# Optimization experiments

Hardware: AMD Instinct MI355X
Metric: run time of the kernel (lower is better)

Reference implementation:

```python
import jax, jax.numpy as jnp
import numpy as np

KEY_DIM = 64
DENSE_DIM = 128
B, N, M = 8, 2048, 256


def setup_inputs() -> dict:
    key = jax.random.key(0)
    ks = jax.random.split(key, 10)
    s_in = 1.0 / np.sqrt(M)
    s_k = 1.0 / np.sqrt(KEY_DIM)
    s_d = 1.0 / np.sqrt(DENSE_DIM)
    return {
        "x": jax.random.normal(ks[0], (B, N, M), dtype=jnp.float32),
        "Wq": jax.random.normal(ks[1], (M, KEY_DIM), dtype=jnp.float32) * s_in,
        "Wk": jax.random.normal(ks[2], (M, KEY_DIM), dtype=jnp.float32) * s_in,
        "Wv": jax.random.normal(ks[3], (M, KEY_DIM), dtype=jnp.float32) * s_in,
        "W1": jax.random.normal(ks[4], (KEY_DIM, DENSE_DIM), dtype=jnp.float32) * s_k,
        "b1": jnp.zeros((DENSE_DIM,), dtype=jnp.float32),
        "W2": jax.random.normal(ks[5], (DENSE_DIM, DENSE_DIM), dtype=jnp.float32) * s_d,
        "b2": jnp.zeros((DENSE_DIM,), dtype=jnp.float32),
        "W3": jax.random.normal(ks[6], (DENSE_DIM, DENSE_DIM), dtype=jnp.float32) * s_d,
        "b3": jnp.zeros((DENSE_DIM,), dtype=jnp.float32),
    }


def reference(x, Wq, Wk, Wv, W1, b1, W2, b2, W3, b3):
    scale = np.sqrt(KEY_DIM).astype(np.float32)
    q = jnp.einsum('bnm,mk->bnk', x, Wq)
    k = jnp.einsum('bnm,mk->bnk', x, Wk)
    v = jnp.einsum('bnm,mk->bnk', x, Wv)
    scores = jnp.einsum('bik,bjk->bij', q, k) / scale  # [B, N, N]
    weights = jax.nn.softmax(scores, axis=-1)
    z = jnp.einsum('bij,bjk->bik', weights, v)  # [B, N, key_dim]
    h = jax.nn.elu(z @ W1 + b1)
    h = jax.nn.elu(h @ W2 + b2)
    out = jax.nn.elu(h @ W3 + b3)
    return out
```

## Files before the change

### kernel.cpp

```cpp
#include <hip/hip_runtime.h>
#include <cstdint>
#include <cstddef>

#define B_ 8
#define N_ 2048
#define M_ 256
#define KD 64
#define DD 128
#define BN (B_ * N_)
#define KSPLIT 4
#define KT_PER (N_ / 64 / KSPLIT)

typedef __attribute__((ext_vector_type(8))) short s16x8;
typedef __attribute__((ext_vector_type(4))) float f32x4;
typedef __attribute__((ext_vector_type(4))) unsigned int u32x4;

__device__ __forceinline__ float elu_f(float x) {
    return x > 0.f ? x : (__expf(x) - 1.f);
}

__device__ __forceinline__ unsigned short f2bf(float f) {
    unsigned int u = __float_as_uint(f);
    u = (u + 0x7FFFu + ((u >> 16) & 1u)) >> 16;
    return (unsigned short)u;
}
__device__ __forceinline__ float bf2f(unsigned short h) {
    return __uint_as_float((unsigned int)h << 16);
}
__device__ __forceinline__ unsigned short bflo(float f, unsigned short h) {
    return f2bf(f - bf2f(h));
}
__device__ __forceinline__ unsigned int packw(float f) {
    unsigned short h = f2bf(f);
    unsigned short lo = bflo(f, h);
    return (unsigned int)h | ((unsigned int)lo << 16);
}
__device__ __forceinline__ unsigned int bfpack2(float a, float b) {
    return (unsigned int)f2bf(a) | ((unsigned int)f2bf(b) << 16);
}

__device__ __forceinline__ void unpack8(const unsigned int* ip, s16x8& ahi, s16x8& alo) {
    const uint4 u0 = *reinterpret_cast<const uint4*>(ip);
    const uint4 u1 = *reinterpret_cast<const uint4*>(ip + 4);
    u32x4 hv, lv;
    hv.x = __byte_perm(u0.x, u0.y, 0x5410);
    hv.y = __byte_perm(u0.z, u0.w, 0x5410);
    hv.z = __byte_perm(u1.x, u1.y, 0x5410);
    hv.w = __byte_perm(u1.z, u1.w, 0x5410);
    lv.x = __byte_perm(u0.x, u0.y, 0x7632);
    lv.y = __byte_perm(u0.z, u0.w, 0x7632);
    lv.z = __byte_perm(u1.x, u1.y, 0x7632);
    lv.w = __byte_perm(u1.z, u1.w, 0x7632);
    ahi = __builtin_bit_cast(s16x8, hv);
    alo = __builtin_bit_cast(s16x8, lv);
}

__global__ __launch_bounds__(256)
void pack_kernel(const float* __restrict__ Wq, const float* __restrict__ Wk,
                 const float* __restrict__ Wv, const float* __restrict__ W1,
                 const float* __restrict__ W2, const float* __restrict__ W3,
                 unsigned short* __restrict__ pQh, unsigned short* __restrict__ pQl,
                 unsigned short* __restrict__ pW1h, unsigned short* __restrict__ pW1l,
                 unsigned short* __restrict__ pW2h, unsigned short* __restrict__ pW2l,
                 unsigned short* __restrict__ pW3h, unsigned short* __restrict__ pW3l) {
    const int id = blockIdx.x * 256 + threadIdx.x;
    const float* W;
    unsigned short *ph, *pl;
    int ncol, ct, c, lane, base;
    if (id < 6144) {
        int mat = id >> 11, rem = id & 2047;
        ct = rem >> 9; c = (rem >> 6) & 7; lane = rem & 63;
        W = (mat == 0) ? Wq : (mat == 1) ? Wk : Wv;
        ncol = KD; ph = pQh; pl = pQl;
        base = (((mat * 4 + ct) * 8 + c) * 64 + lane) * 8;
    } else {
        int id2 = id - 6144;
        if (id2 < 1024) {
            ct = id2 >> 7; c = (id2 >> 6) & 1; lane = id2 & 63;
            W = W1; ncol = DD; ph = pW1h; pl = pW1l;
            base = ((ct * 2 + c) * 64 + lane) * 8;
        } else if (id2 < 3072) {
            int id3 = id2 - 1024;
            ct = id3 >> 8; c = (id3 >> 6) & 3; lane = id3 & 63;
            W = W2; ncol = DD; ph = pW2h; pl = pW2l;
            base = ((ct * 4 + c) * 64 + lane) * 8;
        } else {
            int id3 = id2 - 3072;
            ct = id3 >> 8; c = (id3 >> 6) & 3; lane = id3 & 63;
            W = W3; ncol = DD; ph = pW3h; pl = pW3l;
            base = ((ct * 4 + c) * 64 + lane) * 8;
        }
    }
    const int col = ct * 16 + (lane & 15);
    const int kb = c * 32 + (lane >> 4) * 8;
    #pragma unroll
    for (int j = 0; j < 8; ++j) {
        float v = W[(size_t)(kb + j) * ncol + col];
        unsigned short h = f2bf(v);
        ph[base + j] = h;
        pl[base + j] = bflo(v, h);
    }
}

__global__ __launch_bounds__(256)
void qkv_kernel(const float* __restrict__ x,
                const unsigned short* __restrict__ pQh,
                unsigned short* __restrict__ qb, unsigned short* __restrict__ kb,
                unsigned short* __restrict__ vtb) {
    __shared__ unsigned short xh[32 * 264];
    __shared__ float dbuf[32 * 204];
    const int t = threadIdx.x;
    const int row0 = blockIdx.x * 32;

    for (int i = t; i < 2048; i += 256) {
        int rr = i >> 6, c4 = i & 63;
        float4 v = reinterpret_cast<const float4*>(x + (size_t)(row0 + rr) * M_)[c4];
        ushort4 o;
        o.x = f2bf(v.x); o.y = f2bf(v.y); o.z = f2bf(v.z); o.w = f2bf(v.w);
        *reinterpret_cast<ushort4*>(&xh[rr * 264 + c4 * 4]) = o;
    }
    __syncthreads();

    const int w = t >> 6, l = t & 63, g = l >> 4, r = l & 15;
    const int t0 = 3 * w, t1 = 3 * w + 1, t2 = 3 * w + 2;

    f32x4 acc[3][2];
    #pragma unroll
    for (int m = 0; m < 3; ++m)
        #pragma unroll
        for (int s = 0; s < 2; ++s)
            acc[m][s] = (f32x4){0.f, 0.f, 0.f, 0.f};

    #pragma unroll
    for (int c = 0; c < 8; ++c) {
        const s16x8 a0 = *reinterpret_cast<const s16x8*>(&xh[r * 264 + c * 32 + g * 8]);
        const s16x8 a1 = *reinterpret_cast<const s16x8*>(&xh[(16 + r) * 264 + c * 32 + g * 8]);
        const s16x8 b0 = *reinterpret_cast<const s16x8*>(pQh + ((t0 * 8 + c) * 64 + l) * 8);
        const s16x8 b1 = *reinterpret_cast<const s16x8*>(pQh + ((t1 * 8 + c) * 64 + l) * 8);
        const s16x8 b2 = *reinterpret_cast<const s16x8*>(pQh + ((t2 * 8 + c) * 64 + l) * 8);
        acc[0][0] = __builtin_amdgcn_mfma_f32_16x16x32_bf16(a0, b0, acc[0][0], 0, 0, 0);
        acc[0][1] = __builtin_amdgcn_mfma_f32_16x16x32_bf16(a1, b0, acc[0][1], 0, 0, 0);
        acc[1][0] = __builtin_amdgcn_mfma_f32_16x16x32_bf16(a0, b1, acc[1][0], 0, 0, 0);
        acc[1][1] = __builtin_amdgcn_mfma_f32_16x16x32_bf16(a1, b1, acc[1][1], 0, 0, 0);
        acc[2][0] = __builtin_amdgcn_mfma_f32_16x16x32_bf16(a0, b2, acc[2][0], 0, 0, 0);
        acc[2][1] = __builtin_amdgcn_mfma_f32_16x16x32_bf16(a1, b2, acc[2][1], 0, 0, 0);
    }

    {
        const int c0 = (t0 >> 2) * 68 + (t0 & 3) * 16 + r;
        const int c1 = (t1 >> 2) * 68 + (t1 & 3) * 16 + r;
        const int c2 = (t2 >> 2) * 68 + (t2 & 3) * 16 + r;
        #pragma unroll
        for (int s = 0; s < 2; ++s)
            #pragma unroll
            for (int reg = 0; reg < 4; ++reg) {
                const int rw = (s * 16 + 4 * g + reg) * 204;
                dbuf[rw + c0] = acc[0][s][reg];
                dbuf[rw + c1] = acc[1][s][reg];
                dbuf[rw + c2] = acc[2][s][reg];
            }
    }
    __syncthreads();

    const int b = row0 >> 11, n0 = row0 & 2047;
    {
        const int mat = t >> 7, rem = t & 127, rr = rem >> 2, cq = rem & 3;
        const float* src = &dbuf[rr * 204 + mat * 68 + cq * 16];
        float4 v0 = *reinterpret_cast<const float4*>(src);
        float4 v1 = *reinterpret_cast<const float4*>(src + 4);
        float4 v2 = *reinterpret_cast<const float4*>(src + 8);
        float4 v3 = *reinterpret_cast<const float4*>(src + 12);
        const float sc = (mat == 0) ? 0.125f : 1.0f;
        uint4 o0, o1;
        o0.x = bfpack2(v0.x * sc, v0.y * sc);
        o0.y = bfpack2(v0.z * sc, v0.w * sc);
        o0.z = bfpack2(v1.x * sc, v1.y * sc);
        o0.w = bfpack2(v1.z * sc, v1.w * sc);
        o1.x = bfpack2(v2.x * sc, v2.y * sc);
        o1.y = bfpack2(v2.z * sc, v2.w * sc);
        o1.z = bfpack2(v3.x * sc, v3.y * sc);
        o1.w = bfpack2(v3.z * sc, v3.w * sc);
        unsigned short* dst = (mat == 0 ? qb : kb) + (size_t)(row0 + rr) * KD + cq * 16;
        *reinterpret_cast<uint4*>(dst)     = o0;
        *reinterpret_cast<uint4*>(dst + 8) = o1;
    }
    {
        const int d = t >> 2, ng = (t & 3) * 8;
        unsigned short tmp[8];
        #pragma unroll
        for (int i = 0; i < 8; ++i)
            tmp[i] = f2bf(dbuf[(ng + i) * 204 + 136 + d]);
        uint4 o0;
        o0.x = (unsigned)tmp[0] | ((unsigned)tmp[1] << 16);
        o0.y = (unsigned)tmp[2] | ((unsigned)tmp[3] << 16);
        o0.z = (unsigned)tmp[4] | ((unsigned)tmp[5] << 16);
        o0.w = (unsigned)tmp[6] | ((unsigned)tmp[7] << 16);
        *reinterpret_cast<uint4*>(vtb + ((size_t)b * KD + d) * N_ + n0 + ng) = o0;
    }
}

__global__ __launch_bounds__(128)
void attn_kernel(const unsigned short* __restrict__ qb,
                 const unsigned short* __restrict__ kb,
                 const unsigned short* __restrict__ vtb,
                 float* __restrict__ Zp, float* __restrict__ lsum) {
    __shared__ __align__(16) unsigned short ks[64 * 72];
    __shared__ __align__(16) unsigned short vt[64 * 72];
    __shared__ __align__(16) unsigned short ps[2 * 32 * 72];

    const int t = threadIdx.x;
    const int w = t >> 6;
    const int l = t & 63;
    const int g = l >> 4;
    const int r = l & 15;
    const int bid = blockIdx.x;
    const int split = bid & 3;
    const int qt = (bid >> 2) & 31;
    const int bb = bid >> 7;
    const int qrow0 = qt * 64 + w * 32;
    const int k0 = split * (N_ / KSPLIT);

    const unsigned short* qrowA = qb + ((size_t)bb * N_ + qrow0 + r) * KD + g * 8;
    const unsigned short* qrowB = qrowA + (size_t)16 * KD;
    const s16x8 qfA0 = *reinterpret_cast<const s16x8*>(qrowA);
    const s16x8 qfA1 = *reinterpret_cast<const s16x8*>(qrowA + 32);
    const s16x8 qfB0 = *reinterpret_cast<const s16x8*>(qrowB);
    const s16x8 qfB1 = *reinterpret_cast<const s16x8*>(qrowB + 32);

    const unsigned short* kbase = kb + ((size_t)bb * N_ + k0) * KD;
    const unsigned short* vbase = vtb + (size_t)bb * KD * N_ + k0;
    unsigned short* psw = ps + w * (32 * 72);

    for (int c = t; c < 512; c += 128) {
        int key = c >> 3, sub = c & 7;
        *reinterpret_cast<s16x8*>(&ks[key * 72 + sub * 8]) =
            *reinterpret_cast<const s16x8*>(kbase + (size_t)key * KD + sub * 8);
        *reinterpret_cast<s16x8*>(&vt[key * 72 + sub * 8]) =
            *reinterpret_cast<const s16x8*>(vbase + (size_t)key * N_ + sub * 8);
    }
    __syncthreads();

    f32x4 zacA0 = {0.f,0.f,0.f,0.f}, zacA1 = {0.f,0.f,0.f,0.f};
    f32x4 zacA2 = {0.f,0.f,0.f,0.f}, zacA3 = {0.f,0.f,0.f,0.f};
    f32x4 zacB0 = {0.f,0.f,0.f,0.f}, zacB1 = {0.f,0.f,0.f,0.f};
    f32x4 zacB2 = {0.f,0.f,0.f,0.f}, zacB3 = {0.f,0.f,0.f,0.f};
    float laccA[4] = {0.f, 0.f, 0.f, 0.f};
    float laccB[4] = {0.f, 0.f, 0.f, 0.f};

    for (int kt = 0; kt < KT_PER; ++kt) {
        s16x8 kr[4], vr[4];
        const bool pf = (kt + 1 < KT_PER);
        if (pf) {
            const unsigned short* kg = kbase + (size_t)(kt + 1) * 64 * KD;
            const unsigned short* vg = vbase + (size_t)(kt + 1) * 64;
            #pragma unroll
            for (int i = 0; i < 4; ++i) {
                const int c = t + 128 * i, key = c >> 3, sub = c & 7;
                kr[i] = *reinterpret_cast<const s16x8*>(kg + (size_t)key * KD + sub * 8);
                vr[i] = *reinterpret_cast<const s16x8*>(vg + (size_t)key * N_ + sub * 8);
            }
        }

        f32x4 sA0 = {0.f,0.f,0.f,0.f}, sA1 = {0.f,0.f,0.f,0.f};
        f32x4 sA2 = {0.f,0.f,0.f,0.f}, sA3 = {0.f,0.f,0.f,0.f};
        f32x4 sB0 = {0.f,0.f,0.f,0.f}, sB1 = {0.f,0.f,0.f,0.f};
        f32x4 sB2 = {0.f,0.f,0.f,0.f}, sB3 = {0.f,0.f,0.f,0.f};
        {
            const s16x8 kf00 = *reinterpret_cast<const s16x8*>(&ks[(r +  0) * 72 + g * 8]);
            const s16x8 kf01 = *reinterpret_cast<const s16x8*>(&ks[(r +  0) * 72 + g * 8 + 32]);
            const s16x8 kf10 = *reinterpret_cast<const s16x8*>(&ks[(r + 16) * 72 + g * 8]);
            const s16x8 kf11 = *reinterpret_cast<const s16x8*>(&ks[(r + 16) * 72 + g * 8 + 32]);
            const s16x8 kf20 = *reinterpret_cast<const s16x8*>(&ks[(r + 32) * 72 + g * 8]);
            const s16x8 kf21 = *reinterpret_cast<const s16x8*>(&ks[(r + 32) * 72 + g * 8 + 32]);
            const s16x8 kf30 = *reinterpret_cast<const s16x8*>(&ks[(r + 48) * 72 + g * 8]);
            const s16x8 kf31 = *reinterpret_cast<const s16x8*>(&ks[(r + 48) * 72 + g * 8 + 32]);
            sA0 = __builtin_amdgcn_mfma_f32_16x16x32_bf16(qfA0, kf00, sA0, 0, 0, 0);
            sA0 = __builtin_amdgcn_mfma_f32_16x16x32_bf16(qfA1, kf01, sA0, 0, 0, 0);
            sA1 = __builtin_amdgcn_mfma_f32_16x16x32_bf16(qfA0, kf10, sA1, 0, 0, 0);
            sA1 = __builtin_amdgcn_mfma_f32_16x16x32_bf16(qfA1, kf11, sA1, 0, 0, 0);
            sA2 = __builtin_amdgcn_mfma_f32_16x16x32_bf16(qfA0, kf20, sA2, 0, 0, 0);
            sA2 = __builtin_amdgcn_mfma_f32_16x16x32_bf16(qfA1, kf21, sA2, 0, 0, 0);
            sA3 = __builtin_amdgcn_mfma_f32_16x16x32_bf16(qfA0, kf30, sA3, 0, 0, 0);
            sA3 = __builtin_amdgcn_mfma_f32_16x16x32_bf16(qfA1, kf31, sA3, 0, 0, 0);
            sB0 = __builtin_amdgcn_mfma_f32_16x16x32_bf16(qfB0, kf00, sB0, 0, 0, 0);
            sB0 = __builtin_amdgcn_mfma_f32_16x16x32_bf16(qfB1, kf01, sB0, 0, 0, 0);
            sB1 = __builtin_amdgcn_mfma_f32_16x16x32_bf16(qfB0, kf10, sB1, 0, 0, 0);
            sB1 = __builtin_amdgcn_mfma_f32_16x16x32_bf16(qfB1, kf11, sB1, 0, 0, 0);
            sB2 = __builtin_amdgcn_mfma_f32_16x16x32_bf16(qfB0, kf20, sB2, 0, 0, 0);
            sB2 = __builtin_amdgcn_mfma_f32_16x16x32_bf16(qfB1, kf21, sB2, 0, 0, 0);
            sB3 = __builtin_amdgcn_mfma_f32_16x16x32_bf16(qfB0, kf30, sB3, 0, 0, 0);
            sB3 = __builtin_amdgcn_mfma_f32_16x16x32_bf16(qfB1, kf31, sB3, 0, 0, 0);
        }

        const s16x8 vf00 = *reinterpret_cast<const s16x8*>(&vt[(r +  0) * 72 + g * 8]);
        const s16x8 vf01 = *reinterpret_cast<const s16x8*>(&vt[(r +  0) * 72 + g * 8 + 32]);
        const s16x8 vf10 = *reinterpret_cast<const s16x8*>(&vt[(r + 16) * 72 + g * 8]);
        const s16x8 vf11 = *reinterpret_cast<const s16x8*>(&vt[(r + 16) * 72 + g * 8 + 32]);
        const s16x8 vf20 = *reinterpret_cast<const s16x8*>(&vt[(r + 32) * 72 + g * 8]);
        const s16x8 vf21 = *reinterpret_cast<const s16x8*>(&vt[(r + 32) * 72 + g * 8 + 32]);
        const s16x8 vf30 = *reinterpret_cast<const s16x8*>(&vt[(r + 48) * 72 + g * 8]);
        const s16x8 vf31 = *reinterpret_cast<const s16x8*>(&vt[(r + 48) * 72 + g * 8 + 32]);

        #pragma unroll
        for (int j = 0; j < 4; ++j) {
            float p0 = __expf(sA0[j]);
            float p1 = __expf(sA1[j]);
            float p2 = __expf(sA2[j]);
            float p3 = __expf(sA3[j]);
            laccA[j] += (p0 + p1) + (p2 + p3);
            psw[(4 * g + j) * 72 + r +  0] = f2bf(p0);
            psw[(4 * g + j) * 72 + r + 16] = f2bf(p1);
            psw[(4 * g + j) * 72 + r + 32] = f2bf(p2);
            psw[(4 * g + j) * 72 + r + 48] = f2bf(p3);
        }
        #pragma unroll
        for (int j = 0; j < 4; ++j) {
            float p0 = __expf(sB0[j]);
            float p1 = __expf(sB1[j]);
            float p2 = __expf(sB2[j]);
            float p3 = __expf(sB3[j]);
            laccB[j] += (p0 + p1) + (p2 + p3);
            psw[(16 + 4 * g + j) * 72 + r +  0] = f2bf(p0);
            psw[(16 + 4 * g + j) * 72 + r + 16] = f2bf(p1);
            psw[(16 + 4 * g + j) * 72 + r + 32] = f2bf(p2);
            psw[(16 + 4 * g + j) * 72 + r + 48] = f2bf(p3);
        }

        asm volatile("s_waitcnt lgkmcnt(0)" ::: "memory");
        __builtin_amdgcn_sched_barrier(0);

        const s16x8 paA0 = *reinterpret_cast<const s16x8*>(&psw[r * 72 + g * 8]);
        const s16x8 paA1 = *reinterpret_cast<const s16x8*>(&psw[r * 72 + g * 8 + 32]);
        const s16x8 paB0 = *reinterpret_cast<const s16x8*>(&psw[(16 + r) * 72 + g * 8]);
        const s16x8 paB1 = *reinterpret_cast<const s16x8*>(&psw[(16 + r) * 72 + g * 8 + 32]);
        zacA0 = __builtin_amdgcn_mfma_f32_16x16x32_bf16(paA0, vf00, zacA0, 0, 0, 0);
        zacA0 = __builtin_amdgcn_mfma_f32_16x16x32_bf16(paA1, vf01, zacA0, 0, 0, 0);
        zacA1 = __builtin_amdgcn_mfma_f32_16x16x32_bf16(paA0, vf10, zacA1, 0, 0, 0);
        zacA1 = __builtin_amdgcn_mfma_f32_16x16x32_bf16(paA1, vf11, zacA1, 0, 0, 0);
        zacA2 = __builtin_amdgcn_mfma_f32_16x16x32_bf16(paA0, vf20, zacA2, 0, 0, 0);
        zacA2 = __builtin_amdgcn_mfma_f32_16x16x32_bf16(paA1, vf21, zacA2, 0, 0, 0);
        zacA3 = __builtin_amdgcn_mfma_f32_16x16x32_bf16(paA0, vf30, zacA3, 0, 0, 0);
        zacA3 = __builtin_amdgcn_mfma_f32_16x16x32_bf16(paA1, vf31, zacA3, 0, 0, 0);
        zacB0 = __builtin_amdgcn_mfma_f32_16x16x32_bf16(paB0, vf00, zacB0, 0, 0, 0);
        zacB0 = __builtin_amdgcn_mfma_f32_16x16x32_bf16(paB1, vf01, zacB0, 0, 0, 0);
        zacB1 = __builtin_amdgcn_mfma_f32_16x16x32_bf16(paB0, vf10, zacB1, 0, 0, 0);
        zacB1 = __builtin_amdgcn_mfma_f32_16x16x32_bf16(paB1, vf11, zacB1, 0, 0, 0);
        zacB2 = __builtin_amdgcn_mfma_f32_16x16x32_bf16(paB0, vf20, zacB2, 0, 0, 0);
        zacB2 = __builtin_amdgcn_mfma_f32_16x16x32_bf16(paB1, vf21, zacB2, 0, 0, 0);
        zacB3 = __builtin_amdgcn_mfma_f32_16x16x32_bf16(paB0, vf30, zacB3, 0, 0, 0);
        zacB3 = __builtin_amdgcn_mfma_f32_16x16x32_bf16(paB1, vf31, zacB3, 0, 0, 0);

        __syncthreads();
        if (pf) {
            #pragma unroll
            for (int i = 0; i < 4; ++i) {
                const int c = t + 128 * i, key = c >> 3, sub = c & 7;
                *reinterpret_cast<s16x8*>(&ks[key * 72 + sub * 8]) = kr[i];
                *reinterpret_cast<s16x8*>(&vt[key * 72 + sub * 8]) = vr[i];
            }
        }
        __syncthreads();
    }

    const size_t rowbase = (size_t)split * BN + (size_t)bb * N_ + qrow0;
    #pragma unroll
    for (int j = 0; j < 4; ++j) {
        float lt = laccA[j];
        lt += __shfl_xor(lt, 1);
        lt += __shfl_xor(lt, 2);
        lt += __shfl_xor(lt, 4);
        lt += __shfl_xor(lt, 8);
        if (r == 0)
            lsum[rowbase + 4 * g + j] = lt;
        float* zr = Zp + (rowbase + 4 * g + j) * KD + r;
        zr[ 0] = zacA0[j];
        zr[16] = zacA1[j];
        zr[32] = zacA2[j];
        zr[48] = zacA3[j];
    }
    #pragma unroll
    for (int j = 0; j < 4; ++j) {
        float lt = laccB[j];
        lt += __shfl_xor(lt, 1);
        lt += __shfl_xor(lt, 2);
        lt += __shfl_xor(lt, 4);
        lt += __shfl_xor(lt, 8);
        if (r == 0)
            lsum[rowbase + 16 + 4 * g + j] = lt;
        float* zr = Zp + (rowbase + 16 + 4 * g + j) * KD + r;
        zr[ 0] = zacB0[j];
        zr[16] = zacB1[j];
        zr[32] = zacB2[j];
        zr[48] = zacB3[j];
    }
}

__global__ __launch_bounds__(256)
void mlp_kernel(const float* __restrict__ Zp, const float* __restrict__ lsum,
                const unsigned short* __restrict__ pW1h, const unsigned short* __restrict__ pW1l,
                const unsigned short* __restrict__ pW2h, const unsigned short* __restrict__ pW2l,
                const unsigned short* __restrict__ pW3h, const unsigned short* __restrict__ pW3l,
                const float* __restrict__ b1, const float* __restrict__ b2,
                const float* __restrict__ b3, float* __restrict__ out) {
    __shared__ unsigned int zW[32 * 68];
    __shared__ unsigned int hW[32 * 140];
    const int t = threadIdx.x;
    const int row0 = blockIdx.x * 32;

    {
        const int rr = t >> 3, c8 = (t & 7) * 8;
        const size_t grow = (size_t)row0 + rr;
        const float inv = 1.0f / (lsum[grow] + lsum[BN + grow] +
                                  lsum[2 * (size_t)BN + grow] + lsum[3 * (size_t)BN + grow]);
        const size_t off = grow * KD + c8;
        uint4 wv0, wv1;
        {
            float4 a0 = *reinterpret_cast<const float4*>(Zp + off);
            float4 a1 = *reinterpret_cast<const float4*>(Zp + (size_t)BN * KD + off);
            float4 a2 = *reinterpret_cast<const float4*>(Zp + 2 * (size_t)BN * KD + off);
            float4 a3 = *reinterpret_cast<const float4*>(Zp + 3 * (size_t)BN * KD + off);
            wv0.x = packw((a0.x + a1.x + a2.x + a3.x) * inv);
            wv0.y = packw((a0.y + a1.y + a2.y + a3.y) * inv);
            wv0.z = packw((a0.z + a1.z + a2.z + a3.z) * inv);
            wv0.w = packw((a0.w + a1.w + a2.w + a3.w) * inv);
        }
        {
            float4 a0 = *reinterpret_cast<const float4*>(Zp + off + 4);
            float4 a1 = *reinterpret_cast<const float4*>(Zp + (size_t)BN * KD + off + 4);
            float4 a2 = *reinterpret_cast<const float4*>(Zp + 2 * (size_t)BN * KD + off + 4);
            float4 a3 = *reinterpret_cast<const float4*>(Zp + 3 * (size_t)BN * KD + off + 4);
            wv1.x = packw((a0.x + a1.x + a2.x + a3.x) * inv);
            wv1.y = packw((a0.y + a1.y + a2.y + a3.y) * inv);
            wv1.z = packw((a0.z + a1.z + a2.z + a3.z) * inv);
            wv1.w = packw((a0.w + a1.w + a2.w + a3.w) * inv);
        }
        *reinterpret_cast<uint4*>(&zW[rr * 68 + c8])     = wv0;
        *reinterpret_cast<uint4*>(&zW[rr * 68 + c8 + 4]) = wv1;
    }
    __syncthreads();

    const int w = t >> 6, l = t & 63, g = l >> 4, r = l & 15;
    const int ctA = 2 * w, ctB = 2 * w + 1;

    f32x4 aA[2], aB[2];
    #pragma unroll
    for (int s = 0; s < 2; ++s) { aA[s] = (f32x4){0,0,0,0}; aB[s] = (f32x4){0,0,0,0}; }
    #pragma unroll
    for (int c = 0; c < 2; ++c) {
        s16x8 h0, l0, h1, l1;
        unpack8(&zW[r * 68 + c * 32 + g * 8], h0, l0);
        unpack8(&zW[(16 + r) * 68 + c * 32 + g * 8], h1, l1);
        const int baseA = ((ctA * 2 + c) * 64 + l) * 8;
        const int baseB = ((ctB * 2 + c) * 64 + l) * 8;
        const s16x8 bhA = *reinterpret_cast<const s16x8*>(pW1h + baseA);
        const s16x8 blA = *reinterpret_cast<const s16x8*>(pW1l + baseA);
        const s16x8 bhB = *reinterpret_cast<const s16x8*>(pW1h + baseB);
        const s16x8 blB = *reinterpret_cast<const s16x8*>(pW1l + baseB);
        aA[0] = __builtin_amdgcn_mfma_f32_16x16x32_bf16(h0, bhA, aA[0], 0, 0, 0);
        aA[0] = __builtin_amdgcn_mfma_f32_16x16x32_bf16(h0, blA, aA[0], 0, 0, 0);
        aA[0] = __builtin_amdgcn_mfma_f32_16x16x32_bf16(l0, bhA, aA[0], 0, 0, 0);
        aA[1] = __builtin_amdgcn_mfma_f32_16x16x32_bf16(h1, bhA, aA[1], 0, 0, 0);
        aA[1] = __builtin_amdgcn_mfma_f32_16x16x32_bf16(h1, blA, aA[1], 0, 0, 0);
        aA[1] = __builtin_amdgcn_mfma_f32_16x16x32_bf16(l1, bhA, aA[1], 0, 0, 0);
        aB[0] = __builtin_amdgcn_mfma_f32_16x16x32_bf16(h0, bhB, aB[0], 0, 0, 0);
        aB[0] = __builtin_amdgcn_mfma_f32_16x16x32_bf16(h0, blB, aB[0], 0, 0, 0);
        aB[0] = __builtin_amdgcn_mfma_f32_16x16x32_bf16(l0, bhB, aB[0], 0, 0, 0);
        aB[1] = __builtin_amdgcn_mfma_f32_16x16x32_bf16(h1, bhB, aB[1], 0, 0, 0);
        aB[1] = __builtin_amdgcn_mfma_f32_16x16x32_bf16(h1, blB, aB[1], 0, 0, 0);
        aB[1] = __builtin_amdgcn_mfma_f32_16x16x32_bf16(l1, bhB, aB[1], 0, 0, 0);
    }
    {
        const float bvA = b1[ctA * 16 + r], bvB = b1[ctB * 16 + r];
        #pragma unroll
        for (int s = 0; s < 2; ++s)
            #pragma unroll
            for (int reg = 0; reg < 4; ++reg) {
                const int rw = (s * 16 + 4 * g + reg) * 140;
                hW[rw + ctA * 16 + r] = packw(elu_f(aA[s][reg] + bvA));
                hW[rw + ctB * 16 + r] = packw(elu_f(aB[s][reg] + bvB));
            }
    }
    __syncthreads();

    #pragma unroll
    for (int s = 0; s < 2; ++s) { aA[s] = (f32x4){0,0,0,0}; aB[s] = (f32x4){0,0,0,0}; }
    #pragma unroll
    for (int c = 0; c < 4; ++c) {
        s16x8 h0, l0, h1, l1;
        unpack8(&hW[r * 140 + c * 32 + g * 8], h0, l0);
        unpack8(&hW[(16 + r) * 140 + c * 32 + g * 8], h1, l1);
        const int baseA = ((ctA * 4 + c) * 64 + l) * 8;
        const int baseB = ((ctB * 4 + c) * 64 + l) * 8;
        const s16x8 bhA = *reinterpret_cast<const s16x8*>(pW2h + baseA);
        const s16x8 blA = *reinterpret_cast<const s16x8*>(pW2l + baseA);
        const s16x8 bhB = *reinterpret_cast<const s16x8*>(pW2h + baseB);
        const s16x8 blB = *reinterpret_cast<const s16x8*>(pW2l + baseB);
        aA[0] = __builtin_amdgcn_mfma_f32_16x16x32_bf16(h0, bhA, aA[0], 0, 0, 0);
        aA[0] = __builtin_amdgcn_mfma_f32_16x16x32_bf16(h0, blA, aA[0], 0, 0, 0);
        aA[0] = __builtin_amdgcn_mfma_f32_16x16x32_bf16(l0, bhA, aA[0], 0, 0, 0);
        aA[1] = __builtin_amdgcn_mfma_f32_16x16x32_bf16(h1, bhA, aA[1], 0, 0, 0);
        aA[1] = __builtin_amdgcn_mfma_f32_16x16x32_bf16(h1, blA, aA[1], 0, 0, 0);
        aA[1] = __builtin_amdgcn_mfma_f32_16x16x32_bf16(l1, bhA, aA[1], 0, 0, 0);
        aB[0] = __builtin_amdgcn_mfma_f32_16x16x32_bf16(h0, bhB, aB[0], 0, 0, 0);
        aB[0] = __builtin_amdgcn_mfma_f32_16x16x32_bf16(h0, blB, aB[0], 0, 0, 0);
        aB[0] = __builtin_amdgcn_mfma_f32_16x16x32_bf16(l0, bhB, aB[0], 0, 0, 0);
        aB[1] = __builtin_amdgcn_mfma_f32_16x16x32_bf16(h1, bhB, aB[1], 0, 0, 0);
        aB[1] = __builtin_amdgcn_mfma_f32_16x16x32_bf16(h1, blB, aB[1], 0, 0, 0);
        aB[1] = __builtin_amdgcn_mfma_f32_16x16x32_bf16(l1, bhB, aB[1], 0, 0, 0);
    }
    __syncthreads();
    {
        const float bvA = b2[ctA * 16 + r], bvB = b2[ctB * 16 + r];
        #pragma unroll
        for (int s = 0; s < 2; ++s)
            #pragma unroll
            for (int reg = 0; reg < 4; ++reg) {
                const int rw = (s * 16 + 4 * g + reg) * 140;
                hW[rw + ctA * 16 + r] = packw(elu_f(aA[s][reg] + bvA));
                hW[rw + ctB * 16 + r] = packw(elu_f(aB[s][reg] + bvB));
            }
    }
    __syncthreads();

    #pragma unroll
    for (int s = 0; s < 2; ++s) { aA[s] = (f32x4){0,0,0,0}; aB[s] = (f32x4){0,0,0,0}; }
    #pragma unroll
    for (int c = 0; c < 4; ++c) {
        s16x8 h0, l0, h1, l1;
        unpack8(&hW[r * 140 + c * 32 + g * 8], h0, l0);
        unpack8(&hW[(16 + r) * 140 + c * 32 + g * 8], h1, l1);
        const int baseA = ((ctA * 4 + c) * 64 + l) * 8;
        const int baseB = ((ctB * 4 + c) * 64 + l) * 8;
        const s16x8 bhA = *reinterpret_cast<const s16x8*>(pW3h + baseA);
        const s16x8 blA = *reinterpret_cast<const s16x8*>(pW3l + baseA);
        const s16x8 bhB = *reinterpret_cast<const s16x8*>(pW3h + baseB);
        const s16x8 blB = *reinterpret_cast<const s16x8*>(pW3l + baseB);
        aA[0] = __builtin_amdgcn_mfma_f32_16x16x32_bf16(h0, bhA, aA[0], 0, 0, 0);
        aA[0] = __builtin_amdgcn_mfma_f32_16x16x32_bf16(h0, blA, aA[0], 0, 0, 0);
        aA[0] = __builtin_amdgcn_mfma_f32_16x16x32_bf16(l0, bhA, aA[0], 0, 0, 0);
        aA[1] = __builtin_amdgcn_mfma_f32_16x16x32_bf16(h1, bhA, aA[1], 0, 0, 0);
        aA[1] = __builtin_amdgcn_mfma_f32_16x16x32_bf16(h1, blA, aA[1], 0, 0, 0);
        aA[1] = __builtin_amdgcn_mfma_f32_16x16x32_bf16(l1, bhA, aA[1], 0, 0, 0);
        aB[0] = __builtin_amdgcn_mfma_f32_16x16x32_bf16(h0, bhB, aB[0], 0, 0, 0);
        aB[0] = __builtin_amdgcn_mfma_f32_16x16x32_bf16(h0, blB, aB[0], 0, 0, 0);
        aB[0] = __builtin_amdgcn_mfma_f32_16x16x32_bf16(l0, bhB, aB[0], 0, 0, 0);
        aB[1] = __builtin_amdgcn_mfma_f32_16x16x32_bf16(h1, bhB, aB[1], 0, 0, 0);
        aB[1] = __builtin_amdgcn_mfma_f32_16x16x32_bf16(h1, blB, aB[1], 0, 0, 0);
        aB[1] = __builtin_amdgcn_mfma_f32_16x16x32_bf16(l1, bhB, aB[1], 0, 0, 0);
    }
    {
        const float bvA = b3[ctA * 16 + r], bvB = b3[ctB * 16 + r];
        #pragma unroll
        for (int s = 0; s < 2; ++s)
            #pragma unroll
            for (int reg = 0; reg < 4; ++reg) {
                float* orow = out + (size_t)(row0 + s * 16 + 4 * g + reg) * DD;
                orow[ctA * 16 + r] = elu_f(aA[s][reg] + bvA);
                orow[ctB * 16 + r] = elu_f(aB[s][reg] + bvB);
            }
    }
}

extern "C" void kernel_launch(void* const* d_in, const int* in_sizes, int n_in,
                              void* d_out, int out_size, void* d_ws, size_t ws_size,
                              hipStream_t stream) {
    (void)in_sizes; (void)n_in; (void)out_size; (void)ws_size;
    const float* x  = (const float*)d_in[0];
    const float* Wq = (const float*)d_in[1];
    const float* Wk = (const float*)d_in[2];
    const float* Wv = (const float*)d_in[3];
    const float* W1 = (const float*)d_in[4];
    const float* b1 = (const float*)d_in[5];
    const float* W2 = (const float*)d_in[6];
    const float* b2 = (const float*)d_in[7];
    const float* W3 = (const float*)d_in[8];
    const float* b3 = (const float*)d_in[9];
    float* out = (float*)d_out;

    const size_t nt = (size_t)BN * KD;
    unsigned short* qbf = (unsigned short*)d_ws;
    unsigned short* kbf = qbf + nt;
    unsigned short* vtb = kbf + nt;
    float* Zp   = (float*)(vtb + nt);
    float* lsum = Zp + (size_t)KSPLIT * nt;
    unsigned short* pQh  = (unsigned short*)(lsum + (size_t)KSPLIT * BN);
    unsigned short* pQl  = pQh + 49152;
    unsigned short* pW1h = pQl + 49152;
    unsigned short* pW1l = pW1h + 8192;
    unsigned short* pW2h = pW1l + 8192;
    unsigned short* pW2l = pW2h + 16384;
    unsigned short* pW3h = pW2l + 16384;
    unsigned short* pW3l = pW3h + 16384;

    pack_kernel<<<dim3(44), 256, 0, stream>>>(Wq, Wk, Wv, W1, W2, W3,
                                              pQh, pQl, pW1h, pW1l, pW2h, pW2l, pW3h, pW3l);
    qkv_kernel<<<dim3(BN / 32), 256, 0, stream>>>(x, pQh, qbf, kbf, vtb);
    attn_kernel<<<dim3(BN / 64 * KSPLIT), 128, 0, stream>>>(qbf, kbf, vtb, Zp, lsum);
    mlp_kernel<<<dim3(BN / 32), 256, 0, stream>>>(Zp, lsum, pW1h, pW1l, pW2h, pW2l,
                                                  pW3h, pW3l, b1, b2, b3, out);
}
```

Before: 55.02 us.

## Keep softmax probabilities in registers via transposed QK^T and store bf16 partials

The QK^T MFMA operands are swapped so each lane's score accumulator already matches the A-operand layout needed for the PV MFMA. The probabilities are packed to bf16 in registers instead of going through a shared-memory round trip. The V tile is stored with a permuted column slot order to match this register layout. The split-K partial Z outputs are written as bf16 rather than fp32, halving partial-sum traffic into the MLP kernel, at the cost of some precision in the accumulated partials.

```diff
diff --git a/kernel.cpp b/kernel.cpp
--- a/kernel.cpp
+++ b/kernel.cpp
@@ -38,6 +38,8 @@
 __device__ __forceinline__ unsigned int bfpack2(float a, float b) {
     return (unsigned int)f2bf(a) | ((unsigned int)f2bf(b) << 16);
 }
+__device__ __forceinline__ float bflo32(unsigned int u) { return __uint_as_float(u << 16); }
+__device__ __forceinline__ float bfhi32(unsigned int u) { return __uint_as_float(u & 0xffff0000u); }
 
 __device__ __forceinline__ void unpack8(const unsigned int* ip, s16x8& ahi, s16x8& alo) {
     const uint4 u0 = *reinterpret_cast<const uint4*>(ip);
@@ -203,10 +205,9 @@
 void attn_kernel(const unsigned short* __restrict__ qb,
                  const unsigned short* __restrict__ kb,
                  const unsigned short* __restrict__ vtb,
-                 float* __restrict__ Zp, float* __restrict__ lsum) {
+                 unsigned short* __restrict__ Zp, float* __restrict__ lsum) {
     __shared__ __align__(16) unsigned short ks[64 * 72];
     __shared__ __align__(16) unsigned short vt[64 * 72];
-    __shared__ __align__(16) unsigned short ps[2 * 32 * 72];
 
     const int t = threadIdx.x;
     const int w = t >> 6;
@@ -229,14 +230,16 @@
 
     const unsigned short* kbase = kb + ((size_t)bb * N_ + k0) * KD;
     const unsigned short* vbase = vtb + (size_t)bb * KD * N_ + k0;
-    unsigned short* psw = ps + w * (32 * 72);
 
     for (int c = t; c < 512; c += 128) {
-        int key = c >> 3, sub = c & 7;
-        *reinterpret_cast<s16x8*>(&ks[key * 72 + sub * 8]) =
-            *reinterpret_cast<const s16x8*>(kbase + (size_t)key * KD + sub * 8);
-        *reinterpret_cast<s16x8*>(&vt[key * 72 + sub * 8]) =
-            *reinterpret_cast<const s16x8*>(vbase + (size_t)key * N_ + sub * 8);
+        const int row = c >> 3, sub = c & 7;
+        *reinterpret_cast<s16x8*>(&ks[row * 72 + sub * 8]) =
+            *reinterpret_cast<const s16x8*>(kbase + (size_t)row * KD + sub * 8);
+        const s16x8 vv = *reinterpret_cast<const s16x8*>(vbase + (size_t)row * N_ + sub * 8);
+        const u32x4 vw = __builtin_bit_cast(u32x4, vv);
+        const int slot = 32 * (sub >> 2) + 16 * (sub & 1) + 4 * ((sub >> 1) & 1);
+        *reinterpret_cast<uint2*>(&vt[row * 72 + slot])     = make_uint2(vw.x, vw.y);
+        *reinterpret_cast<uint2*>(&vt[row * 72 + slot + 8]) = make_uint2(vw.z, vw.w);
     }
     __syncthreads();
 
@@ -244,8 +247,7 @@
     f32x4 zacA2 = {0.f,0.f,0.f,0.f}, zacA3 = {0.f,0.f,0.f,0.f};
     f32x4 zacB0 = {0.f,0.f,0.f,0.f}, zacB1 = {0.f,0.f,0.f,0.f};
     f32x4 zacB2 = {0.f,0.f,0.f,0.f}, zacB3 = {0.f,0.f,0.f,0.f};
-    float laccA[4] = {0.f, 0.f, 0.f, 0.f};
-    float laccB[4] = {0.f, 0.f, 0.f, 0.f};
+    float laccA = 0.f, laccB = 0.f;
 
     for (int kt = 0; kt < KT_PER; ++kt) {
         s16x8 kr[4], vr[4];
@@ -255,16 +257,15 @@
             const unsigned short* vg = vbase + (size_t)(kt + 1) * 64;
             #pragma unroll
             for (int i = 0; i < 4; ++i) {
-                const int c = t + 128 * i, key = c >> 3, sub = c & 7;
-                kr[i] = *reinterpret_cast<const s16x8*>(kg + (size_t)key * KD + sub * 8);
-                vr[i] = *reinterpret_cast<const s16x8*>(vg + (size_t)key * N_ + sub * 8);
+                const int c = t + 128 * i, row = c >> 3, sub = c & 7;
+                kr[i] = *reinterpret_cast<const s16x8*>(kg + (size_t)row * KD + sub * 8);
+                vr[i] = *reinterpret_cast<const s16x8*>(vg + (size_t)row * N_ + sub * 8);
             }
         }
 
-        f32x4 sA0 = {0.f,0.f,0.f,0.f}, sA1 = {0.f,0.f,0.f,0.f};
-        f32x4 sA2 = {0.f,0.f,0.f,0.f}, sA3 = {0.f,0.f,0.f,0.f};
-        f32x4 sB0 = {0.f,0.f,0.f,0.f}, sB1 = {0.f,0.f,0.f,0.f};
-        f32x4 sB2 = {0.f,0.f,0.f,0.f}, sB3 = {0.f,0.f,0.f,0.f};
+        f32x4 sA[4], sB[4];
+        #pragma unroll
+        for (int i = 0; i < 4; ++i) { sA[i] = (f32x4){0,0,0,0}; sB[i] = (f32x4){0,0,0,0}; }
         {
             const s16x8 kf00 = *reinterpret_cast<const s16x8*>(&ks[(r +  0) * 72 + g * 8]);
             const s16x8 kf01 = *reinterpret_cast<const s16x8*>(&ks[(r +  0) * 72 + g * 8 + 32]);
@@ -274,23 +275,53 @@
             const s16x8 kf21 = *reinterpret_cast<const s16x8*>(&ks[(r + 32) * 72 + g * 8 + 32]);
             const s16x8 kf30 = *reinterpret_cast<const s16x8*>(&ks[(r + 48) * 72 + g * 8]);
             const s16x8 kf31 = *reinterpret_cast<const s16x8*>(&ks[(r + 48) * 72 + g * 8 + 32]);
-            sA0 = __builtin_amdgcn_mfma_f32_16x16x32_bf16(qfA0, kf00, sA0, 0, 0, 0);
-            sA0 = __builtin_amdgcn_mfma_f32_16x16x32_bf16(qfA1, kf01, sA0, 0, 0, 0);
-            sA1 = __builtin_amdgcn_mfma_f32_16x16x32_bf16(qfA0, kf10, sA1, 0, 0, 0);
-            sA1 = __builtin_amdgcn_mfma_f32_16x16x32_bf16(qfA1, kf11, sA1, 0, 0, 0);
-            sA2 = __builtin_amdgcn_mfma_f32_16x16x32_bf16(qfA0, kf20, sA2, 0, 0, 0);
-            sA2 = __builtin_amdgcn_mfma_f32_16x16x32_bf16(qfA1, kf21, sA2, 0, 0, 0);
-            sA3 = __builtin_amdgcn_mfma_f32_16x16x32_bf16(qfA0, kf30, sA3, 0, 0, 0);
-            sA3 = __builtin_amdgcn_mfma_f32_16x16x32_bf16(qfA1, kf31, sA3, 0, 0, 0);
-            sB0 = __builtin_amdgcn_mfma_f32_16x16x32_bf16(qfB0, kf00, sB0, 0, 0, 0);
-            sB0 = __builtin_amdgcn_mfma_f32_16x16x32_bf16(qfB1, kf01, sB0, 0, 0, 0);
-            sB1 = __builtin_amdgcn_mfma_f32_16x16x32_bf16(qfB0, kf10, sB1, 0, 0, 0);
-            sB1 = __builtin_amdgcn_mfma_f32_16x16x32_bf16(qfB1, kf11, sB1, 0, 0, 0);
-            sB2 = __builtin_amdgcn_mfma_f32_16x16x32_bf16(qfB0, kf20, sB2, 0, 0, 0);
-            sB2 = __builtin_amdgcn_mfma_f32_16x16x32_bf16(qfB1, kf21, sB2, 0, 0, 0);
-            sB3 = __builtin_amdgcn_mfma_f32_16x16x32_bf16(qfB0, kf30, sB3, 0, 0, 0);
-            sB3 = __builtin_amdgcn_mfma_f32_16x16x32_bf16(qfB1, kf31, sB3, 0, 0, 0);
-        }
+            sA[0] = __builtin_amdgcn_mfma_f32_16x16x32_bf16(kf00, qfA0, sA[0], 0, 0, 0);
+            sA[0] = __builtin_amdgcn_mfma_f32_16x16x32_bf16(kf01, qfA1, sA[0], 0, 0, 0);
+            sA[1] = __builtin_amdgcn_mfma_f32_16x16x32_bf16(kf10, qfA0, sA[1], 0, 0, 0);
+            sA[1] = __builtin_amdgcn_mfma_f32_16x16x32_bf16(kf11, qfA1, sA[1], 0, 0, 0);
+            sA[2] = __builtin_amdgcn_mfma_f32_16x16x32_bf16(kf20, qfA0, sA[2], 0, 0, 0);
+            sA[2] = __builtin_amdgcn_mfma_f32_16x16x32_bf16(kf21, qfA1, sA[2], 0, 0, 0);
+            sA[3] = __builtin_amdgcn_mfma_f32_16x16x32_bf16(kf30, qfA0, sA[3], 0, 0, 0);
+            sA[3] = __builtin_amdgcn_mfma_f32_16x16x32_bf16(kf31, qfA1, sA[3], 0, 0, 0);
+            sB[0] = __builtin_amdgcn_mfma_f32_16x16x32_bf16(kf00, qfB0, sB[0], 0, 0, 0);
+            sB[0] = __builtin_amdgcn_mfma_f32_16x16x32_bf16(kf01, qfB1, sB[0], 0, 0, 0);
+            sB[1] = __builtin_amdgcn_mfma_f32_16x16x32_bf16(kf10, qfB0, sB[1], 0, 0, 0);
+            sB[1] = __builtin_amdgcn_mfma_f32_16x16x32_bf16(kf11, qfB1, sB[1], 0, 0, 0);
+            sB[2] = __builtin_amdgcn_mfma_f32_16x16x32_bf16(kf20, qfB0, sB[2], 0, 0, 0);
+            sB[2] = __builtin_amdgcn_mfma_f32_16x16x32_bf16(kf21, qfB1, sB[2], 0, 0, 0);
+            sB[3] = __builtin_amdgcn_mfma_f32_16x16x32_bf16(kf30, qfB0, sB[3], 0, 0, 0);
+            sB[3] = __builtin_amdgcn_mfma_f32_16x16x32_bf16(kf31, qfB1, sB[3], 0, 0, 0);
+        }
+
+        unsigned int wA[8], wB[8];
+        #pragma unroll
+        for (int tt = 0; tt < 4; ++tt) {
+            float p0 = __expf(sA[tt][0]);
+            float p1 = __expf(sA[tt][1]);
+            float p2 = __expf(sA[tt][2]);
+            float p3 = __expf(sA[tt][3]);
+            laccA += (p0 + p1) + (p2 + p3);
+            wA[2 * tt]     = bfpack2(p0, p1);
+            wA[2 * tt + 1] = bfpack2(p2, p3);
+        }
+        #pragma unroll
+        for (int tt = 0; tt < 4; ++tt) {
+            float p0 = __expf(sB[tt][0]);
+            float p1 = __expf(sB[tt][1]);
+            float p2 = __expf(sB[tt][2]);
+            float p3 = __expf(sB[tt][3]);
+            laccB += (p0 + p1) + (p2 + p3);
+            wB[2 * tt]     = bfpack2(p0, p1);
+            wB[2 * tt + 1] = bfpack2(p2, p3);
+        }
+        u32x4 pwA0 = {wA[0], wA[1], wA[2], wA[3]};
+        u32x4 pwA1 = {wA[4], wA[5], wA[6], wA[7]};
+        u32x4 pwB0 = {wB[0], wB[1], wB[2], wB[3]};
+        u32x4 pwB1 = {wB[4], wB[5], wB[6], wB[7]};
+        const s16x8 paA0 = __builtin_bit_cast(s16x8, pwA0);
+        const s16x8 paA1 = __builtin_bit_cast(s16x8, pwA1);
+        const s16x8 paB0 = __builtin_bit_cast(s16x8, pwB0);
+        const s16x8 paB1 = __builtin_bit_cast(s16x8, pwB1);
 
         const s16x8 vf00 = *reinterpret_cast<const s16x8*>(&vt[(r +  0) * 72 + g * 8]);
         const s16x8 vf01 = *reinterpret_cast<const s16x8*>(&vt[(r +  0) * 72 + g * 8 + 32]);
@@ -301,38 +332,6 @@
         const s16x8 vf30 = *reinterpret_cast<const s16x8*>(&vt[(r + 48) * 72 + g * 8]);
         const s16x8 vf31 = *reinterpret_cast<const s16x8*>(&vt[(r + 48) * 72 + g * 8 + 32]);
 
-        #pragma unroll
-        for (int j = 0; j < 4; ++j) {
-            float p0 = __expf(sA0[j]);
-            float p1 = __expf(sA1[j]);
-            float p2 = __expf(sA2[j]);
-            float p3 = __expf(sA3[j]);
-            laccA[j] += (p0 + p1) + (p2 + p3);
-            psw[(4 * g + j) * 72 + r +  0] = f2bf(p0);
-            psw[(4 * g + j) * 72 + r + 16] = f2bf(p1);
-            psw[(4 * g + j) * 72 + r + 32] = f2bf(p2);
-            psw[(4 * g + j) * 72 + r + 48] = f2bf(p3);
-        }
-        #pragma unroll
-        for (int j = 0; j < 4; ++j) {
-            float p0 = __expf(sB0[j]);
-            float p1 = __expf(sB1[j]);
-            float p2 = __expf(sB2[j]);
-            float p3 = __expf(sB3[j]);
-            laccB[j] += (p0 + p1) + (p2 + p3);
-            psw[(16 + 4 * g + j) * 72 + r +  0] = f2bf(p0);
-            psw[(16 + 4 * g + j) * 72 + r + 16] = f2bf(p1);
-            psw[(16 + 4 * g + j) * 72 + r + 32] = f2bf(p2);
-            psw[(16 + 4 * g + j) * 72 + r + 48] = f2bf(p3);
-        }
-
-        asm volatile("s_waitcnt lgkmcnt(0)" ::: "memory");
-        __builtin_amdgcn_sched_barrier(0);
-
-        const s16x8 paA0 = *reinterpret_cast<const s16x8*>(&psw[r * 72 + g * 8]);
-        const s16x8 paA1 = *reinterpret_cast<const s16x8*>(&psw[r * 72 + g * 8 + 32]);
-        const s16x8 paB0 = *reinterpret_cast<const s16x8*>(&psw[(16 + r) * 72 + g * 8]);
-        const s16x8 paB1 = *reinterpret_cast<const s16x8*>(&psw[(16 + r) * 72 + g * 8 + 32]);
         zacA0 = __builtin_amdgcn_mfma_f32_16x16x32_bf16(paA0, vf00, zacA0, 0, 0, 0);
         zacA0 = __builtin_amdgcn_mfma_f32_16x16x32_bf16(paA1, vf01, zacA0, 0, 0, 0);
         zacA1 = __builtin_amdgcn_mfma_f32_16x16x32_bf16(paA0, vf10, zacA1, 0, 0, 0);
@@ -354,49 +353,47 @@
         if (pf) {
             #pragma unroll
             for (int i = 0; i < 4; ++i) {
-                const int c = t + 128 * i, key = c >> 3, sub = c & 7;
-                *reinterpret_cast<s16x8*>(&ks[key * 72 + sub * 8]) = kr[i];
-                *reinterpret_cast<s16x8*>(&vt[key * 72 + sub * 8]) = vr[i];
+                const int c = t + 128 * i, row = c >> 3, sub = c & 7;
+                *reinterpret_cast<s16x8*>(&ks[row * 72 + sub * 8]) = kr[i];
+                const u32x4 vw = __builtin_bit_cast(u32x4, vr[i]);
+                const int slot = 32 * (sub >> 2) + 16 * (sub & 1) + 4 * ((sub >> 1) & 1);
+                *reinterpret_cast<uint2*>(&vt[row * 72 + slot])     = make_uint2(vw.x, vw.y);
+                *reinterpret_cast<uint2*>(&vt[row * 72 + slot + 8]) = make_uint2(vw.z, vw.w);
             }
         }
         __syncthreads();
     }
 
     const size_t rowbase = (size_t)split * BN + (size_t)bb * N_ + qrow0;
-    #pragma unroll
-    for (int j = 0; j < 4; ++j) {
-        float lt = laccA[j];
-        lt += __shfl_xor(lt, 1);
-        lt += __shfl_xor(lt, 2);
-        lt += __shfl_xor(lt, 4);
-        lt += __shfl_xor(lt, 8);
-        if (r == 0)
-            lsum[rowbase + 4 * g + j] = lt;
-        float* zr = Zp + (rowbase + 4 * g + j) * KD + r;
-        zr[ 0] = zacA0[j];
-        zr[16] = zacA1[j];
-        zr[32] = zacA2[j];
-        zr[48] = zacA3[j];
-    }
-    #pragma unroll
-    for (int j = 0; j < 4; ++j) {
-        float lt = laccB[j];
-        lt += __shfl_xor(lt, 1);
-        lt += __shfl_xor(lt, 2);
-        lt += __shfl_xor(lt, 4);
-        lt += __shfl_xor(lt, 8);
-        if (r == 0)
-            lsum[rowbase + 16 + 4 * g + j] = lt;
-        float* zr = Zp + (rowbase + 16 + 4 * g + j) * KD + r;
-        zr[ 0] = zacB0[j];
-        zr[16] = zacB1[j];
-        zr[32] = zacB2[j];
-        zr[48] = zacB3[j];
+    {
+        float ltA = laccA;
+        ltA += __shfl_xor(ltA, 16);
+        ltA += __shfl_xor(ltA, 32);
+        float ltB = laccB;
+        ltB += __shfl_xor(ltB, 16);
+        ltB += __shfl_xor(ltB, 32);
+        if (l < 16) {
+            lsum[rowbase + r]      = ltA;
+            lsum[rowbase + 16 + r] = ltB;
+        }
+    }
+    #pragma unroll
+    for (int reg = 0; reg < 4; ++reg) {
+        unsigned short* zrA = Zp + (rowbase + 4 * g + reg) * KD + r;
+        zrA[ 0] = f2bf(zacA0[reg]);
+        zrA[16] = f2bf(zacA1[reg]);
+        zrA[32] = f2bf(zacA2[reg]);
+        zrA[48] = f2bf(zacA3[reg]);
+        unsigned short* zrB = Zp + (rowbase + 16 + 4 * g + reg) * KD + r;
+        zrB[ 0] = f2bf(zacB0[reg]);
+        zrB[16] = f2bf(zacB1[reg]);
+        zrB[32] = f2bf(zacB2[reg]);
+        zrB[48] = f2bf(zacB3[reg]);
     }
 }
 
 __global__ __launch_bounds__(256)
-void mlp_kernel(const float* __restrict__ Zp, const float* __restrict__ lsum,
+void mlp_kernel(const unsigned short* __restrict__ Zp, const float* __restrict__ lsum,
                 const unsigned short* __restrict__ pW1h, const unsigned short* __restrict__ pW1l,
                 const unsigned short* __restrict__ pW2h, const unsigned short* __restrict__ pW2l,
                 const unsigned short* __restrict__ pW3h, const unsigned short* __restrict__ pW3l,
@@ -413,29 +410,27 @@
         const float inv = 1.0f / (lsum[grow] + lsum[BN + grow] +
                                   lsum[2 * (size_t)BN + grow] + lsum[3 * (size_t)BN + grow]);
         const size_t off = grow * KD + c8;
-        uint4 wv0, wv1;
-        {
-            float4 a0 = *reinterpret_cast<const float4*>(Zp + off);
-            float4 a1 = *reinterpret_cast<const float4*>(Zp + (size_t)BN * KD + off);
-            float4 a2 = *reinterpret_cast<const float4*>(Zp + 2 * (size_t)BN * KD + off);
-            float4 a3 = *reinterpret_cast<const float4*>(Zp + 3 * (size_t)BN * KD + off);
-            wv0.x = packw((a0.x + a1.x + a2.x + a3.x) * inv);
-            wv0.y = packw((a0.y + a1.y + a2.y + a3.y) * inv);
-            wv0.z = packw((a0.z + a1.z + a2.z + a3.z) * inv);
-            wv0.w = packw((a0.w + a1.w + a2.w + a3.w) * inv);
-        }
-        {
-            float4 a0 = *reinterpret_cast<const float4*>(Zp + off + 4);
-            float4 a1 = *reinterpret_cast<const float4*>(Zp + (size_t)BN * KD + off + 4);
-            float4 a2 = *reinterpret_cast<const float4*>(Zp + 2 * (size_t)BN * KD + off + 4);
-            float4 a3 = *reinterpret_cast<const float4*>(Zp + 3 * (size_t)BN * KD + off + 4);
-            wv1.x = packw((a0.x + a1.x + a2.x + a3.x) * inv);
-            wv1.y = packw((a0.y + a1.y + a2.y + a3.y) * inv);
-            wv1.z = packw((a0.z + a1.z + a2.z + a3.z) * inv);
-            wv1.w = packw((a0.w + a1.w + a2.w + a3.w) * inv);
-        }
-        *reinterpret_cast<uint4*>(&zW[rr * 68 + c8])     = wv0;
-        *reinterpret_cast<uint4*>(&zW[rr * 68 + c8 + 4]) = wv1;
+        const uint4 z0 = *reinterpret_cast<const uint4*>(Zp + off);
+        const uint4 z1 = *reinterpret_cast<const uint4*>(Zp + (size_t)BN * KD + off);
+        const uint4 z2 = *reinterpret_cast<const uint4*>(Zp + 2 * (size_t)BN * KD + off);
+        const uint4 z3 = *reinterpret_cast<const uint4*>(Zp + 3 * (size_t)BN * KD + off);
+        const unsigned int a0[4] = {z0.x, z0.y, z0.z, z0.w};
+        const unsigned int a1[4] = {z1.x, z1.y, z1.z, z1.w};
+        const unsigned int a2[4] = {z2.x, z2.y, z2.z, z2.w};
+        const unsigned int a3[4] = {z3.x, z3.y, z3.z, z3.w};
+        unsigned int ww[8];
+        #pragma unroll
+        for (int i = 0; i < 4; ++i) {
+            float lo = bflo32(a0[i]) + bflo32(a1[i]) + bflo32(a2[i]) + bflo32(a3[i]);
+            float hi = bfhi32(a0[i]) + bfhi32(a1[i]) + bfhi32(a2[i]) + bfhi32(a3[i]);
+            ww[2 * i]     = packw(lo * inv);
+            ww[2 * i + 1] = packw(hi * inv);
+        }
+        uint4 o0, o1;
+        o0.x = ww[0]; o0.y = ww[1]; o0.z = ww[2]; o0.w = ww[3];
+        o1.x = ww[4]; o1.y = ww[5]; o1.z = ww[6]; o1.w = ww[7];
+        *reinterpret_cast<uint4*>(&zW[rr * 68 + c8])     = o0;
+        *reinterpret_cast<uint4*>(&zW[rr * 68 + c8 + 4]) = o1;
     }
     __syncthreads();
 
@@ -581,8 +576,8 @@
     unsigned short* qbf = (unsigned short*)d_ws;
     unsigned short* kbf = qbf + nt;
     unsigned short* vtb = kbf + nt;
-    float* Zp   = (float*)(vtb + nt);
-    float* lsum = Zp + (size_t)KSPLIT * nt;
+    unsigned short* Zp  = vtb + nt;
+    float* lsum = (float*)(Zp + (size_t)KSPLIT * nt);
     unsigned short* pQh  = (unsigned short*)(lsum + (size_t)KSPLIT * BN);
     unsigned short* pQl  = pQh + 49152;
     unsigned short* pW1h = pQl + 49152;
```

Result: faster. 52.16 us (median of 2 runs) (-5.2%).
